# Kernel optimization log

Hardware: AMD Instinct MI355X
Metric: run time of the kernel (lower is better)

## Reference

```python
import jax, jax.numpy as jnp
import numpy as np

B, H, W, C_IN, C_QK = 8, 64, 64, 256, 32


def setup_inputs() -> dict:
    key = jax.random.key(0)
    ks = jax.random.split(key, 5)
    x = jax.random.normal(ks[0], (B, H, W, C_IN), dtype=jnp.float32)
    Wq = jax.random.normal(ks[1], (C_IN, C_QK), dtype=jnp.float32) * 0.05
    bq = jnp.zeros((C_QK,), dtype=jnp.float32)
    Wk = jax.random.normal(ks[2], (C_IN, C_QK), dtype=jnp.float32) * 0.05
    bk = jnp.zeros((C_QK,), dtype=jnp.float32)
    Wv = jax.random.normal(ks[3], (C_IN, C_IN), dtype=jnp.float32) * 0.05
    bv = jnp.zeros((C_IN,), dtype=jnp.float32)
    gamma = jax.random.normal(ks[4], (1,), dtype=jnp.float32)
    return {"x": x, "Wq": Wq, "bq": bq, "Wk": Wk, "bk": bk, "Wv": Wv, "bv": bv, "gamma": gamma}


def reference(x, Wq, bq, Wk, bk, Wv, bv, gamma):
    b, h, w, c_in = x.shape
    n = h * w
    xt = x.reshape(b, n, c_in)                      # tokens: (B, N, C_in)
    # 1x1 convs == per-token channel matmuls
    q = xt @ Wq + bq                                # (B, N, Cqk)
    k = xt @ Wk + bk                                # (B, N, Cqk)
    v = xt @ Wv + bv                                # (B, N, C_in)
    energy = jnp.einsum('bnc,bmc->bnm', q, k)       # (B, N, N)
    attn = jax.nn.softmax(energy, axis=-1)
    # original: out = (V^T @ A^T)^T == A @ V
    out = jnp.einsum('bnm,bmc->bnc', attn, v)       # (B, N, C_in)
    out = out.reshape(b, h, w, c_in)
    out = gamma * out + x                           # residual with learned scale
    return jnp.mean(out, axis=-1)                   # channel-mean pool -> (B, H, W)
```

## Files before the change

### kernel.cpp

```cpp
#include <hip/hip_runtime.h>
#include <hip/hip_bf16.h>


typedef _Float16 half8  __attribute__((ext_vector_type(8)));
typedef _Float16 half4v __attribute__((ext_vector_type(4)));
typedef float    f32x4  __attribute__((ext_vector_type(4)));
typedef float    f32x2  __attribute__((ext_vector_type(2)));

#define LOG2E 1.4426950408889634f

#if __has_builtin(__builtin_amdgcn_exp2f)
#define EXP2(x) __builtin_amdgcn_exp2f(x)
#else
#define EXP2(x) exp2f(x)
#endif

__global__ __launch_bounds__(256) void prep_kernel(
    const float* __restrict__ Wq, const float* __restrict__ Wk,
    const float* __restrict__ Wv, const float* __restrict__ bv,
    _Float16* __restrict__ Wfr, float* __restrict__ wvbar, float* __restrict__ bvbar)
{
  int bid = blockIdx.x, tid = threadIdx.x;
  if (bid < 64) {
    int col = bid, c = tid;
    float v = (col < 32) ? Wq[c * 32 + col] : Wk[c * 32 + (col - 32)];
    int ch = c >> 5, quad = (c >> 3) & 3, j = c & 7;
    Wfr[(size_t)((ch * 4 + quad) * 64 + col) * 8 + j] = (_Float16)v;
  } else if (bid < 128) {
    int row = (bid - 64) * 4 + (tid >> 6);
    int lane = tid & 63;
    const float* p = Wv + (size_t)row * 256 + lane * 4;
    float s = p[0] + p[1] + p[2] + p[3];
    #pragma unroll
    for (int off = 32; off >= 1; off >>= 1) s += __shfl_xor(s, off);
    if (lane == 0) wvbar[row] = s * (1.0f / 256.0f);
  } else {
    if (tid < 64) {
      const float* p = bv + tid * 4;
      float s = p[0] + p[1] + p[2] + p[3];
      #pragma unroll
      for (int off = 32; off >= 1; off >>= 1) s += __shfl_xor(s, off);
      if (tid == 0) bvbar[0] = s * (1.0f / 256.0f);
    }
  }
}

__global__ __launch_bounds__(256) void proj_kernel(
    const float* __restrict__ x, const _Float16* __restrict__ Wfr,
    const float* __restrict__ bq, const float* __restrict__ bk,
    const float* __restrict__ wvbar, const float* __restrict__ bvbar,
    _Float16* __restrict__ Qh, _Float16* __restrict__ Kh,
    float* __restrict__ vbarO, float* __restrict__ xbarO)
{
  __shared__ _Float16 XT[64 * 264];
  int tid = threadIdx.x, blk = blockIdx.x;
  size_t tok0 = (size_t)blk * 64;

  const float4* xg4 = (const float4*)x;
  #pragma unroll
  for (int i = 0; i < 16; ++i) {
    int f = i * 256 + tid;
    int tok = f >> 6, c4 = f & 63;
    float4 v = xg4[(size_t)blk * 4096 + f];
    half4v h;
    h.x = (_Float16)v.x; h.y = (_Float16)v.y; h.z = (_Float16)v.z; h.w = (_Float16)v.w;
    *(half4v*)&XT[tok * 264 + c4 * 4] = h;
  }
  __syncthreads();

  if (tid < 64) {
    float vs = 0.f, xs = 0.f;
    #pragma unroll 4
    for (int g = 0; g < 32; ++g) {
      half8 h = *(const half8*)&XT[tid * 264 + g * 8];
      #pragma unroll
      for (int j = 0; j < 8; ++j) {
        float xv = (float)h[j];
        vs += xv * wvbar[g * 8 + j];
        xs += xv;
      }
    }
    vbarO[tok0 + tid] = vs + bvbar[0];
    xbarO[tok0 + tid] = xs * (1.0f / 256.0f);
  }

  int lane = tid & 63, w = tid >> 6;
  int l15 = lane & 15, quad = lane >> 4;
  f32x4 acc[4] = {(f32x4){0,0,0,0},(f32x4){0,0,0,0},(f32x4){0,0,0,0},(f32x4){0,0,0,0}};
  #pragma unroll
  for (int ch = 0; ch < 8; ++ch) {
    half8 a = *(const half8*)&XT[(w * 16 + l15) * 264 + ch * 32 + quad * 8];
    #pragma unroll
    for (int ct = 0; ct < 4; ++ct) {
      half8 bf = *(const half8*)(Wfr + (size_t)((ch * 4 + quad) * 64 + ct * 16 + l15) * 8);
      acc[ct] = __builtin_amdgcn_mfma_f32_16x16x32_f16(a, bf, acc[ct], 0, 0, 0);
    }
  }
  #pragma unroll
  for (int ct = 0; ct < 4; ++ct) {
    int col = ct * 16 + l15;
    #pragma unroll
    for (int r = 0; r < 4; ++r) {
      int token = w * 16 + quad * 4 + r;
      if (ct < 2) {
        float val = (acc[ct][r] + bq[col]) * LOG2E;
        Qh[(tok0 + token) * 32 + col] = (_Float16)val;
      } else {
        float val = acc[ct][r] + bk[col - 32];
        Kh[(tok0 + token) * 32 + (col - 32)] = (_Float16)val;
      }
    }
  }
}

__global__ __launch_bounds__(256, 4) void flash_kernel(
    const _Float16* __restrict__ Qh, const _Float16* __restrict__ Kh,
    const float* __restrict__ vbar,
    float* __restrict__ lpart, float* __restrict__ opart)
{
  int tid = threadIdx.x, blk = blockIdx.x;
  int ks = blk & 1, qt = (blk >> 1) & 63, b = blk >> 7;
  int lane = tid & 63, w = tid >> 6;
  int l15 = lane & 15, quad = lane >> 4;

  const _Float16* Qb = Qh + (size_t)b * 4096 * 32;
  const _Float16* Kb = Kh + (size_t)b * 4096 * 32 + (size_t)ks * 2048 * 32;
  const float* vb = vbar + (size_t)b * 4096 + ks * 2048;

  int qrow = qt * 64 + w * 16 + l15;
  half8 aq = *(const half8*)(Qb + (size_t)qrow * 32 + quad * 8);

  const f32x4 cinit = {-88.f, -88.f, -88.f, -88.f};
  const _Float16* kfrag = Kb + (size_t)l15 * 32 + quad * 8;
  const float* vfrag = vb + l15;

  f32x2 lacc[4] = {(f32x2){0,0},(f32x2){0,0},(f32x2){0,0},(f32x2){0,0}};
  f32x2 oacc[4] = {(f32x2){0,0},(f32x2){0,0},(f32x2){0,0},(f32x2){0,0}};

  half8 kc0, kc1, kc2, kc3;
  float vc0, vc1, vc2, vc3;
  kc0 = *(const half8*)(kfrag + 0 * 512);
  kc1 = *(const half8*)(kfrag + 1 * 512);
  kc2 = *(const half8*)(kfrag + 2 * 512);
  kc3 = *(const half8*)(kfrag + 3 * 512);
  vc0 = vfrag[0]; vc1 = vfrag[16]; vc2 = vfrag[32]; vc3 = vfrag[48];

  for (int kt = 0; kt < 32; ++kt) {
    half8 kn0, kn1, kn2, kn3;
    float vn0, vn1, vn2, vn3;
    if (kt < 31) {
      const _Float16* kf = kfrag + (size_t)(kt + 1) * 2048;
      const float* vf = vfrag + (kt + 1) * 64;
      kn0 = *(const half8*)(kf + 0 * 512);
      kn1 = *(const half8*)(kf + 1 * 512);
      kn2 = *(const half8*)(kf + 2 * 512);
      kn3 = *(const half8*)(kf + 3 * 512);
      vn0 = vf[0]; vn1 = vf[16]; vn2 = vf[32]; vn3 = vf[48];
    }
    f32x4 s0 = __builtin_amdgcn_mfma_f32_16x16x32_f16(aq, kc0, cinit, 0, 0, 0);
    f32x4 s1 = __builtin_amdgcn_mfma_f32_16x16x32_f16(aq, kc1, cinit, 0, 0, 0);
    f32x4 s2 = __builtin_amdgcn_mfma_f32_16x16x32_f16(aq, kc2, cinit, 0, 0, 0);
    f32x4 s3 = __builtin_amdgcn_mfma_f32_16x16x32_f16(aq, kc3, cinit, 0, 0, 0);
    f32x2 va = {vc0, vc1}, vbp = {vc2, vc3};
    #pragma unroll
    for (int r = 0; r < 4; ++r) {
      f32x2 pa = {EXP2(s0[r]), EXP2(s1[r])};
      f32x2 pb = {EXP2(s2[r]), EXP2(s3[r])};
      lacc[r] += pa + pb;
      oacc[r] += pa * va;
      oacc[r] += pb * vbp;
    }
    kc0 = kn0; kc1 = kn1; kc2 = kn2; kc3 = kn3;
    vc0 = vn0; vc1 = vn1; vc2 = vn2; vc3 = vn3;
  }

  #pragma unroll
  for (int r = 0; r < 4; ++r) {
    float ls = lacc[r].x + lacc[r].y;
    float os = oacc[r].x + oacc[r].y;
    #pragma unroll
    for (int off = 1; off < 16; off <<= 1) {
      ls += __shfl_xor(ls, off);
      os += __shfl_xor(os, off);
    }
    if (l15 == 0) {
      int row = qt * 64 + w * 16 + quad * 4 + r;
      size_t idx = (size_t)ks * 32768 + (size_t)b * 4096 + row;
      lpart[idx] = ls;
      opart[idx] = os;
    }
  }
}

__global__ __launch_bounds__(256) void combine_kernel(
    const float* __restrict__ lpart, const float* __restrict__ opart,
    const float* __restrict__ xbar, const float* __restrict__ gamma,
    float* __restrict__ out)
{
  int i = blockIdx.x * 256 + threadIdx.x;
  float l = lpart[i] + lpart[32768 + i];
  float o = opart[i] + opart[32768 + i];
  out[i] = gamma[0] * (o / l) + xbar[i];
}

extern "C" void kernel_launch(void* const* d_in, const int* in_sizes, int n_in,
                              void* d_out, int out_size, void* d_ws, size_t ws_size,
                              hipStream_t stream)
{
  const float* x     = (const float*)d_in[0];
  const float* Wq    = (const float*)d_in[1];
  const float* bq    = (const float*)d_in[2];
  const float* Wk    = (const float*)d_in[3];
  const float* bk    = (const float*)d_in[4];
  const float* Wv    = (const float*)d_in[5];
  const float* bv    = (const float*)d_in[6];
  const float* gamma = (const float*)d_in[7];
  float* out = (float*)d_out;

  char* ws = (char*)d_ws;
  _Float16* Wfr  = (_Float16*)(ws);
  float* wvbar   = (float*)(ws + 32768);
  float* bvbar   = (float*)(ws + 33792);
  _Float16* Qh   = (_Float16*)(ws + 65536);
  _Float16* Kh   = (_Float16*)(ws + 65536 + 2097152);
  float* vbarA   = (float*)(ws + 65536 + 4194304);
  float* xbarA   = (float*)(ws + 65536 + 4194304 + 131072);
  float* lpart   = (float*)(ws + 65536 + 4194304 + 262144);
  float* opart   = (float*)(ws + 65536 + 4194304 + 524288);

  prep_kernel<<<129, 256, 0, stream>>>(Wq, Wk, Wv, bv, Wfr, wvbar, bvbar);
  proj_kernel<<<512, 256, 0, stream>>>(x, Wfr, bq, bk, wvbar, bvbar, Qh, Kh, vbarA, xbarA);
  flash_kernel<<<1024, 256, 0, stream>>>(Qh, Kh, vbarA, lpart, opart);
  combine_kernel<<<128, 256, 0, stream>>>(lpart, opart, xbarA, gamma, out);
}
```

Before: 128.6 us.

## Fuse combine into flash kernel, drop LDS staging in projection, compute means via MFMA

The projection kernel now loads x straight from global memory into MFMA A fragments, with no LDS transpose or barrier. It computes the per-token V-mean and x-mean with an extra MFMA whose B operand holds the fp16 column means of Wv and a constant 1/256. The flash kernel now uses 512-thread blocks: the two key halves run as separate wave groups in one block and are reduced through shared memory, so the separate combine kernel and its partial buffers are gone. This removes one launch and the LDS staging work, but rounds the Wv mean weights to fp16 and halves the number of flash blocks.

```diff
diff --git a/kernel.cpp b/kernel.cpp
--- a/kernel.cpp
+++ b/kernel.cpp
@@ -3,7 +3,6 @@
 
 
 typedef _Float16 half8  __attribute__((ext_vector_type(8)));
-typedef _Float16 half4v __attribute__((ext_vector_type(4)));
 typedef float    f32x4  __attribute__((ext_vector_type(4)));
 typedef float    f32x2  __attribute__((ext_vector_type(2)));
 
@@ -18,7 +17,8 @@
 __global__ __launch_bounds__(256) void prep_kernel(
     const float* __restrict__ Wq, const float* __restrict__ Wk,
     const float* __restrict__ Wv, const float* __restrict__ bv,
-    _Float16* __restrict__ Wfr, float* __restrict__ wvbar, float* __restrict__ bvbar)
+    _Float16* __restrict__ Wfr, float* __restrict__ wvbar,
+    _Float16* __restrict__ wvbarH, float* __restrict__ bvbar)
 {
   int bid = blockIdx.x, tid = threadIdx.x;
   if (bid < 64) {
@@ -33,7 +33,11 @@
     float s = p[0] + p[1] + p[2] + p[3];
     #pragma unroll
     for (int off = 32; off >= 1; off >>= 1) s += __shfl_xor(s, off);
-    if (lane == 0) wvbar[row] = s * (1.0f / 256.0f);
+    if (lane == 0) {
+      float m = s * (1.0f / 256.0f);
+      wvbar[row] = m;
+      wvbarH[row] = (_Float16)m;
+    }
   } else {
     if (tid < 64) {
       const float* p = bv + tid * 4;
@@ -47,87 +51,94 @@
 
 __global__ __launch_bounds__(256) void proj_kernel(
     const float* __restrict__ x, const _Float16* __restrict__ Wfr,
+    const _Float16* __restrict__ wvbarH,
     const float* __restrict__ bq, const float* __restrict__ bk,
-    const float* __restrict__ wvbar, const float* __restrict__ bvbar,
+    const float* __restrict__ bvbar,
     _Float16* __restrict__ Qh, _Float16* __restrict__ Kh,
     float* __restrict__ vbarO, float* __restrict__ xbarO)
 {
-  __shared__ _Float16 XT[64 * 264];
   int tid = threadIdx.x, blk = blockIdx.x;
-  size_t tok0 = (size_t)blk * 64;
-
-  const float4* xg4 = (const float4*)x;
-  #pragma unroll
-  for (int i = 0; i < 16; ++i) {
-    int f = i * 256 + tid;
-    int tok = f >> 6, c4 = f & 63;
-    float4 v = xg4[(size_t)blk * 4096 + f];
-    half4v h;
-    h.x = (_Float16)v.x; h.y = (_Float16)v.y; h.z = (_Float16)v.z; h.w = (_Float16)v.w;
-    *(half4v*)&XT[tok * 264 + c4 * 4] = h;
-  }
-  __syncthreads();
-
-  if (tid < 64) {
-    float vs = 0.f, xs = 0.f;
-    #pragma unroll 4
-    for (int g = 0; g < 32; ++g) {
-      half8 h = *(const half8*)&XT[tid * 264 + g * 8];
-      #pragma unroll
-      for (int j = 0; j < 8; ++j) {
-        float xv = (float)h[j];
-        vs += xv * wvbar[g * 8 + j];
-        xs += xv;
-      }
-    }
-    vbarO[tok0 + tid] = vs + bvbar[0];
-    xbarO[tok0 + tid] = xs * (1.0f / 256.0f);
-  }
-
   int lane = tid & 63, w = tid >> 6;
   int l15 = lane & 15, quad = lane >> 4;
-  f32x4 acc[4] = {(f32x4){0,0,0,0},(f32x4){0,0,0,0},(f32x4){0,0,0,0},(f32x4){0,0,0,0}};
+  size_t tok0 = (size_t)blk * 64 + w * 16;
+
+  const float* xrow = x + (tok0 + l15) * 256;
+
+  half8 c256h;
+  #pragma unroll
+  for (int j = 0; j < 8; ++j) c256h[j] = (_Float16)(1.0f / 256.0f);
+
+  f32x4 accQ0 = {0,0,0,0}, accQ1 = {0,0,0,0};
+  f32x4 accK0 = {0,0,0,0}, accK1 = {0,0,0,0};
+  f32x4 accS  = {0,0,0,0};
+
   #pragma unroll
   for (int ch = 0; ch < 8; ++ch) {
-    half8 a = *(const half8*)&XT[(w * 16 + l15) * 264 + ch * 32 + quad * 8];
-    #pragma unroll
-    for (int ct = 0; ct < 4; ++ct) {
-      half8 bf = *(const half8*)(Wfr + (size_t)((ch * 4 + quad) * 64 + ct * 16 + l15) * 8);
-      acc[ct] = __builtin_amdgcn_mfma_f32_16x16x32_f16(a, bf, acc[ct], 0, 0, 0);
-    }
-  }
-  #pragma unroll
-  for (int ct = 0; ct < 4; ++ct) {
-    int col = ct * 16 + l15;
-    #pragma unroll
-    for (int r = 0; r < 4; ++r) {
-      int token = w * 16 + quad * 4 + r;
-      if (ct < 2) {
-        float val = (acc[ct][r] + bq[col]) * LOG2E;
-        Qh[(tok0 + token) * 32 + col] = (_Float16)val;
-      } else {
-        float val = acc[ct][r] + bk[col - 32];
-        Kh[(tok0 + token) * 32 + (col - 32)] = (_Float16)val;
-      }
-    }
-  }
-}
-
-__global__ __launch_bounds__(256, 4) void flash_kernel(
+    const float* ap = xrow + ch * 32 + quad * 8;
+    float4 a0 = *(const float4*)ap;
+    float4 a1 = *(const float4*)(ap + 4);
+    half8 a;
+    a[0] = (_Float16)a0.x; a[1] = (_Float16)a0.y;
+    a[2] = (_Float16)a0.z; a[3] = (_Float16)a0.w;
+    a[4] = (_Float16)a1.x; a[5] = (_Float16)a1.y;
+    a[6] = (_Float16)a1.z; a[7] = (_Float16)a1.w;
+
+    const _Float16* wb = Wfr + (size_t)((ch * 4 + quad) * 64 + l15) * 8;
+    half8 b0 = *(const half8*)(wb + 0 * 16 * 8);
+    half8 b1 = *(const half8*)(wb + 1 * 16 * 8);
+    half8 b2 = *(const half8*)(wb + 2 * 16 * 8);
+    half8 b3 = *(const half8*)(wb + 3 * 16 * 8);
+
+    accQ0 = __builtin_amdgcn_mfma_f32_16x16x32_f16(a, b0, accQ0, 0, 0, 0);
+    accQ1 = __builtin_amdgcn_mfma_f32_16x16x32_f16(a, b1, accQ1, 0, 0, 0);
+    accK0 = __builtin_amdgcn_mfma_f32_16x16x32_f16(a, b2, accK0, 0, 0, 0);
+    accK1 = __builtin_amdgcn_mfma_f32_16x16x32_f16(a, b3, accK1, 0, 0, 0);
+
+    half8 wv8 = *(const half8*)(wvbarH + ch * 32 + quad * 8);
+    half8 bs = {0,0,0,0,0,0,0,0};
+    if (l15 == 0) bs = wv8;
+    if (l15 == 1) bs = c256h;
+    accS = __builtin_amdgcn_mfma_f32_16x16x32_f16(a, bs, accS, 0, 0, 0);
+  }
+
+  float bq0 = bq[l15], bq1 = bq[16 + l15];
+  float bk0 = bk[l15], bk1 = bk[16 + l15];
+  #pragma unroll
+  for (int r = 0; r < 4; ++r) {
+    size_t g = tok0 + quad * 4 + r;
+    Qh[g * 32 + l15]      = (_Float16)((accQ0[r] + bq0) * LOG2E);
+    Qh[g * 32 + 16 + l15] = (_Float16)((accQ1[r] + bq1) * LOG2E);
+    Kh[g * 32 + l15]      = (_Float16)(accK0[r] + bk0);
+    Kh[g * 32 + 16 + l15] = (_Float16)(accK1[r] + bk1);
+  }
+  if (l15 == 0) {
+    float bvb = bvbar[0];
+    #pragma unroll
+    for (int r = 0; r < 4; ++r) vbarO[tok0 + quad * 4 + r] = accS[r] + bvb;
+  }
+  if (l15 == 1) {
+    #pragma unroll
+    for (int r = 0; r < 4; ++r) xbarO[tok0 + quad * 4 + r] = accS[r];
+  }
+}
+
+__global__ __launch_bounds__(512, 4) void flash_kernel(
     const _Float16* __restrict__ Qh, const _Float16* __restrict__ Kh,
-    const float* __restrict__ vbar,
-    float* __restrict__ lpart, float* __restrict__ opart)
-{
+    const float* __restrict__ vbar, const float* __restrict__ xbar,
+    const float* __restrict__ gamma, float* __restrict__ out)
+{
+  __shared__ float lsm[2][64], osm[2][64];
   int tid = threadIdx.x, blk = blockIdx.x;
-  int ks = blk & 1, qt = (blk >> 1) & 63, b = blk >> 7;
+  int b = blk >> 6, qt = blk & 63;
   int lane = tid & 63, w = tid >> 6;
+  int qs = w & 3, kh = w >> 2;
   int l15 = lane & 15, quad = lane >> 4;
 
   const _Float16* Qb = Qh + (size_t)b * 4096 * 32;
-  const _Float16* Kb = Kh + (size_t)b * 4096 * 32 + (size_t)ks * 2048 * 32;
-  const float* vb = vbar + (size_t)b * 4096 + ks * 2048;
-
-  int qrow = qt * 64 + w * 16 + l15;
+  const _Float16* Kb = Kh + (size_t)b * 4096 * 32 + (size_t)kh * 2048 * 32;
+  const float* vb = vbar + (size_t)b * 4096 + kh * 2048;
+
+  int qrow = qt * 64 + qs * 16 + l15;
   half8 aq = *(const half8*)(Qb + (size_t)qrow * 32 + quad * 8);
 
   const f32x4 cinit = {-88.f, -88.f, -88.f, -88.f};
@@ -184,23 +195,18 @@
       os += __shfl_xor(os, off);
     }
     if (l15 == 0) {
-      int row = qt * 64 + w * 16 + quad * 4 + r;
-      size_t idx = (size_t)ks * 32768 + (size_t)b * 4096 + row;
-      lpart[idx] = ls;
-      opart[idx] = os;
-    }
-  }
-}
-
-__global__ __launch_bounds__(256) void combine_kernel(
-    const float* __restrict__ lpart, const float* __restrict__ opart,
-    const float* __restrict__ xbar, const float* __restrict__ gamma,
-    float* __restrict__ out)
-{
-  int i = blockIdx.x * 256 + threadIdx.x;
-  float l = lpart[i] + lpart[32768 + i];
-  float o = opart[i] + opart[32768 + i];
-  out[i] = gamma[0] * (o / l) + xbar[i];
+      int rr = qs * 16 + quad * 4 + r;
+      lsm[kh][rr] = ls;
+      osm[kh][rr] = os;
+    }
+  }
+  __syncthreads();
+  if (tid < 64) {
+    float l = lsm[0][tid] + lsm[1][tid];
+    float o = osm[0][tid] + osm[1][tid];
+    size_t idx = (size_t)b * 4096 + qt * 64 + tid;
+    out[idx] = gamma[0] * (o / l) + xbar[idx];
+  }
 }
 
 extern "C" void kernel_launch(void* const* d_in, const int* in_sizes, int n_in,
@@ -218,18 +224,16 @@
   float* out = (float*)d_out;
 
   char* ws = (char*)d_ws;
-  _Float16* Wfr  = (_Float16*)(ws);
-  float* wvbar   = (float*)(ws + 32768);
-  float* bvbar   = (float*)(ws + 33792);
-  _Float16* Qh   = (_Float16*)(ws + 65536);
-  _Float16* Kh   = (_Float16*)(ws + 65536 + 2097152);
-  float* vbarA   = (float*)(ws + 65536 + 4194304);
-  float* xbarA   = (float*)(ws + 65536 + 4194304 + 131072);
-  float* lpart   = (float*)(ws + 65536 + 4194304 + 262144);
-  float* opart   = (float*)(ws + 65536 + 4194304 + 524288);
-
-  prep_kernel<<<129, 256, 0, stream>>>(Wq, Wk, Wv, bv, Wfr, wvbar, bvbar);
-  proj_kernel<<<512, 256, 0, stream>>>(x, Wfr, bq, bk, wvbar, bvbar, Qh, Kh, vbarA, xbarA);
-  flash_kernel<<<1024, 256, 0, stream>>>(Qh, Kh, vbarA, lpart, opart);
-  combine_kernel<<<128, 256, 0, stream>>>(lpart, opart, xbarA, gamma, out);
-}
+  _Float16* Wfr    = (_Float16*)(ws);
+  float* wvbar     = (float*)(ws + 32768);
+  _Float16* wvbarH = (_Float16*)(ws + 33792);
+  float* bvbar     = (float*)(ws + 34304);
+  _Float16* Qh     = (_Float16*)(ws + 65536);
+  _Float16* Kh     = (_Float16*)(ws + 65536 + 2097152);
+  float* vbarA     = (float*)(ws + 65536 + 4194304);
+  float* xbarA     = (float*)(ws + 65536 + 4194304 + 131072);
+
+  prep_kernel<<<129, 256, 0, stream>>>(Wq, Wk, Wv, bv, Wfr, wvbar, wvbarH, bvbar);
+  proj_kernel<<<512, 256, 0, stream>>>(x, Wfr, wvbarH, bq, bk, bvbar, Qh, Kh, vbarA, xbarA);
+  flash_kernel<<<512, 512, 0, stream>>>(Qh, Kh, vbarA, xbarA, gamma, out);
+}
```

New measurement: 127.0 us. Within noise of the previous version (-1.3%).
